# Kernel optimization log

Hardware: AMD Instinct MI355X
Metric: run time of the kernel (lower is better)

## Reference

```python
import jax, jax.numpy as jnp
import numpy as np

DIM = 384
H = 64
W = 64
NB = 8
BS = DIM // NB
WF = W // 2 + 1
EPS = 1e-5


def _layernorm(x, g, b):
    mu = jnp.mean(x, axis=-1, keepdims=True)
    var = jnp.mean(jnp.square(x - mu), axis=-1, keepdims=True)
    return (x - mu) * jax.lax.rsqrt(var + EPS) * g + b


def setup_inputs() -> dict:
    key = jax.random.key(0)
    ks = jax.random.split(key, 8)
    scale = 0.02
    x = jax.random.normal(ks[0], (8, H, W, DIM), dtype=jnp.float32)
    # complex params stored as real view (..., 2) like torch.view_as_real
    w1 = scale * jax.random.normal(ks[1], (H, WF, NB, BS, BS, 2), dtype=jnp.float32)
    b1 = scale * jax.random.normal(ks[2], (H, WF, NB, BS, 2), dtype=jnp.float32)
    norm1_w = jnp.ones((DIM,), jnp.float32)
    norm1_b = jnp.zeros((DIM,), jnp.float32)
    norm2_w = jnp.ones((DIM,), jnp.float32)
    norm2_b = jnp.zeros((DIM,), jnp.float32)
    lim1 = 1.0 / np.sqrt(DIM)
    lim2 = 1.0 / np.sqrt(4 * DIM)
    mlp_w1 = jax.random.uniform(ks[3], (DIM, 4 * DIM), jnp.float32, -lim1, lim1)
    mlp_b1 = jax.random.uniform(ks[4], (4 * DIM,), jnp.float32, -lim1, lim1)
    mlp_w2 = jax.random.uniform(ks[5], (4 * DIM, DIM), jnp.float32, -lim2, lim2)
    mlp_b2 = jax.random.uniform(ks[6], (DIM,), jnp.float32, -lim2, lim2)
    return {"x": x, "w1": w1, "b1": b1, "norm1_w": norm1_w, "norm1_b": norm1_b,
            "norm2_w": norm2_w, "norm2_b": norm2_b, "mlp_w1": mlp_w1, "mlp_b1": mlp_b1,
            "mlp_w2": mlp_w2, "mlp_b2": mlp_b2}


def reference(x, w1, b1, norm1_w, norm1_b, norm2_w, norm2_b, mlp_w1, mlp_b1, mlp_w2, mlp_b2):
    B, h, w, C = x.shape
    residual = x
    xn = _layernorm(x, norm1_w, norm1_b)
    # spectral token mixing (fp32, ortho norm)
    xf = jnp.fft.rfft2(xn.astype(jnp.float32), axes=(1, 2), norm="ortho")  # (B,H,WF,C) complex
    xf = xf.reshape(B, h, w // 2 + 1, NB, BS)
    w1c = jax.lax.complex(w1[..., 0], w1[..., 1])  # (H,WF,NB,BS,BS)
    b1c = jax.lax.complex(b1[..., 0], b1[..., 1])  # (H,WF,NB,BS)
    o1 = jnp.einsum("bhwni,hwnio->bhwno", xf, w1c) + b1c
    o1 = jax.lax.complex(jax.nn.relu(o1.real), jax.nn.relu(o1.imag))
    o1 = o1.reshape(B, h, w // 2 + 1, C)
    xs = jnp.fft.irfft2(o1, s=(h, w), axes=(1, 2), norm="ortho")  # (B,H,W,C) real
    # channel MLP (dropout in eval mode = identity), exact GELU as torch default
    xm = _layernorm(xs, norm2_w, norm2_b)
    hdn = jax.nn.gelu(xm @ mlp_w1 + mlp_b1, approximate=False)
    mlp_out = hdn @ mlp_w2 + mlp_b2
    return xs + residual + mlp_out
```

## Files before the change

### kernel.cpp

```cpp
#include <hip/hip_runtime.h>
#include <math.h>


#define BB 8
#define CC 384
#define WF 33
#define NBK 8
#define BSZ 48
#define NTOK 32768
#define TW64 0.09817477042468103f

#define T_AWF 0
#define T_AHF 5120
#define T_AHI 21504
#define T_AWI 37888

typedef __attribute__((ext_vector_type(8))) short bf16x8;
typedef __attribute__((ext_vector_type(4))) float f32x4;

__device__ __forceinline__ unsigned short f2b(float f) {
  union { float f; unsigned u; } x; x.f = f;
  unsigned u = x.u;
  return (unsigned short)((u + 0x7fffu + ((u >> 16) & 1u)) >> 16);
}
__device__ __forceinline__ float b2fl(unsigned short u) {
  return __uint_as_float(((unsigned)u) << 16);
}
__device__ __forceinline__ void gload16(const void* g, void* l) {
  __builtin_amdgcn_global_load_lds(
      (const __attribute__((address_space(1))) void*)g,
      (__attribute__((address_space(3))) void*)l, 16, 0, 0);
}

__global__ __launch_bounds__(256) void prep_kernel(unsigned short* __restrict__ A,
    const float* __restrict__ mw1, unsigned short* __restrict__ w1t,
    const float* __restrict__ mw2, unsigned short* __restrict__ w2t,
    const float* __restrict__ n2w, const float* __restrict__ n2b,
    const float* __restrict__ mb1, float2* __restrict__ gsbb) {
  __shared__ float tile[32][33];
  int bid = blockIdx.x;
  if (bid < 64) {
    int idx0 = bid * 256 + threadIdx.x;
    const float S = 0.125f;
    for (int e = idx0; e < 5120; e += 16384) {
      int m = e >> 6, w = e & 63;
      float val = 0.f;
      if (m < 66) {
        int kwv = m >> 1;
        float th = (float)((kwv * w) & 63) * TW64;
        val = (m & 1) ? (((kwv==0)||(kwv==32)) ? 0.f : -sinf(th)*S) : cosf(th)*S;
      }
      A[T_AWF + e] = f2b(val);
    }
    for (int e = idx0; e < 16384; e += 16384) {
      int comp = e >> 13; int r = e & 8191; int mp = r >> 6, hh = r & 63;
      int cpo = mp >> 6, kh = mp & 63;
      float th = (float)((kh * hh) & 63) * TW64;
      float cv = cosf(th), sv = sinf(th);
      float fv = (cpo == 0) ? (comp == 0 ? cv : sv) : (comp == 0 ? -sv : cv);
      A[T_AHF + e] = f2b(fv * S);
      float iv = (cpo == 0) ? (comp == 0 ? cv : -sv) : (comp == 0 ? sv : cv);
      A[T_AHI + e] = f2b(iv * S);
    }
    for (int e = idx0; e < 4096; e += 16384) {
      int w = e >> 6, kp = e & 63;
      float val;
      if (kp <= 32) {
        float th = (float)((kp * w) & 63) * TW64;
        val = cosf(th) * (((kp==0)||(kp==32)) ? 1.f : 2.f) * S;
      } else {
        int k2 = kp - 32;
        float th = (float)((k2 * w) & 63) * TW64;
        val = -2.f * sinf(th) * S;
      }
      A[T_AWI + e] = f2b(val);
    }
    return;
  }
  if (bid >= 1216) {
    int n0 = (bid - 1216) * 256 + threadIdx.x;
    if (n0 < 1536) {
      float gsv = 0.f, bbv = 0.f;
      for (int k = 0; k < 384; ++k) {
        float a = mw1[(size_t)k*1536 + n0];
        gsv += n2w[k]*a;
        bbv += n2b[k]*a;
      }
      gsbb[n0] = make_float2(gsv, bbv + mb1[n0]);
    }
    return;
  }
  int tx = threadIdx.x & 31, ty = threadIdx.x >> 5;
  if (bid < 640) {
    int tb = bid - 64;
    int ntc = 1536 >> 5;
    int bx = tb % ntc, by = tb / ntc;
    for (int rr2 = ty; rr2 < 32; rr2 += 8)
      tile[rr2][tx] = mw1[(size_t)(by*32+rr2)*1536 + bx*32 + tx];
    __syncthreads();
    float gv = n2w[by*32 + tx];
    for (int rr2 = ty; rr2 < 32; rr2 += 8)
      w1t[(size_t)(bx*32+rr2)*384 + by*32 + tx] = f2b(tile[tx][rr2] * gv);
  } else {
    int tb = bid - 640;
    int ntc = 384 >> 5;
    int bx = tb % ntc, by = tb / ntc;
    for (int rr2 = ty; rr2 < 32; rr2 += 8)
      tile[rr2][tx] = mw2[(size_t)(by*32+rr2)*384 + bx*32 + tx];
    __syncthreads();
    for (int rr2 = ty; rr2 < 32; rr2 += 8)
      w2t[(size_t)(bx*32+rr2)*1536 + by*32 + tx] = f2b(tile[tx][rr2]);
  }
}

__global__ __launch_bounds__(256) void ln1t_kernel(const float* __restrict__ x,
    const float* __restrict__ g, const float* __restrict__ be,
    unsigned short* __restrict__ xn) {
  int outer = blockIdx.x;
  int tid = threadIdx.x, lane = tid & 63, wg = tid >> 6;
  const float* base = x + (size_t)outer * 64 * 384;
  float s[16], s2[16];
#pragma unroll
  for (int q = 0; q < 16; ++q) { s[q] = 0.f; s2[q] = 0.f; }
  for (int ch = 0; ch < 6; ++ch) {
#pragma unroll
    for (int q = 0; q < 16; ++q) {
      float v = base[(size_t)(wg*16 + q)*384 + ch*64 + lane];
      s[q] += v; s2[q] += v*v;
    }
  }
#pragma unroll
  for (int q = 0; q < 16; ++q) {
#pragma unroll
    for (int off = 32; off >= 1; off >>= 1) {
      s[q] += __shfl_xor(s[q], off);
      s2[q] += __shfl_xor(s2[q], off);
    }
  }
  float mu[16], rs[16];
#pragma unroll
  for (int q = 0; q < 16; ++q) {
    mu[q] = s[q] * (1.f/384.f);
    rs[q] = rsqrtf(s2[q] * (1.f/384.f) - mu[q]*mu[q] + 1e-5f);
  }
  unsigned short* o = xn + (size_t)outer * 384 * 64;
  for (int ch = 0; ch < 6; ++ch) {
    int c = ch*64 + lane;
    float ga = g[c], bb2 = be[c];
#pragma unroll
    for (int qq = 0; qq < 4; ++qq) {
      unsigned short hv[4];
#pragma unroll
      for (int r2 = 0; r2 < 4; ++r2) {
        int q = qq*4 + r2;
        hv[r2] = f2b((base[(size_t)(wg*16+q)*384 + c]-mu[q])*rs[q]*ga + bb2);
      }
      uint2 pw;
      pw.x = hv[0] | ((unsigned)hv[1] << 16);
      pw.y = hv[2] | ((unsigned)hv[3] << 16);
      *(uint2*)(o + (size_t)c*64 + wg*16 + qq*4) = pw;
    }
  }
}

template<int STAGE>
__global__ __launch_bounds__(256) void dft_kernel(
    const unsigned short* __restrict__ A0, const unsigned short* __restrict__ D,
    unsigned short* __restrict__ O) {
  constexpr int M = (STAGE==0) ? 80 : (STAGE==3) ? 64 : 128;
  constexpr int MT = M / 16;
  constexpr int NA = (STAGE==1 || STAGE==2) ? 2 : 1;
  constexpr int ABYTES = NA * M * 128;
  constexpr int STG2 = ABYTES + 16384;
  constexpr int EPB = 64 * 128 * 4;
  constexpr int SB = (STG2 > EPB) ? STG2 : EPB;
  __shared__ __align__(16) char smem[SB];
  char* BPL = smem + ABYTES;

  int bid = blockIdx.x;
  int cc = bid % 3; int outer = bid / 3;
  int c0 = cc * 128;
  int tid = threadIdx.x, lane = tid & 63, wid = tid >> 6;
  int rr = lane & 15, rq = lane >> 4;
  int b, h = 0, kw = 0;
  if (STAGE == 0 || STAGE == 3) { b = outer >> 6; h = outer & 63; }
  else { b = outer / 33; kw = outer % 33; }

  f32x4 acc[MT][2];
#pragma unroll
  for (int mt = 0; mt < MT; ++mt)
#pragma unroll
    for (int nt = 0; nt < 2; ++nt) acc[mt][nt] = (f32x4){0.f,0.f,0.f,0.f};

  const unsigned short* Atab =
    (STAGE==0) ? A0+T_AWF : (STAGE==1) ? A0+T_AHF : (STAGE==2) ? A0+T_AHI : A0+T_AWI;
  constexpr int ACH = NA * M * 8;
#pragma unroll
  for (int i = 0; i < (ACH + 255)/256; ++i) {
    int t2 = tid + i*256;
    if ((ACH % 256 == 0) || (t2 < ACH)) {
      int mm = t2 >> 3, ch = t2 & 7;
      gload16(Atab + mm*64 + ((ch ^ (mm & 7)) << 3), smem + i*4096 + wid*1024);
    }
  }

  int ncomp = (STAGE == 1) ? ((kw == 0 || kw == 32) ? 1 : 2) : NA;

  for (int comp = 0; comp < ncomp; ++comp) {
    if (comp) __syncthreads();
    if (STAGE == 0) {
      const unsigned short* src = D + (((size_t)(b*64 + h))*384 + c0) * 64;
#pragma unroll
      for (int i = 0; i < 4; ++i) {
        int idx = tid + i*256;
        int c = idx >> 3, ch = idx & 7;
        gload16(src + c*64 + ((ch ^ (c & 7)) << 3), BPL + i*4096 + wid*1024);
      }
    } else {
      size_t P; int RS;
      if (STAGE == 1) { P = (size_t)b*(64*66*384) + (size_t)(2*kw + comp)*384 + c0; RS = 66*384; }
      else if (STAGE == 2) { P = ((size_t)((b*2 + comp)*33) + kw)*64*384 + c0; RS = 384; }
      else { P = (size_t)b*(64*64*384) + (size_t)h*384 + c0; RS = 64*384; }
      const unsigned short* p0 = D + P;
#pragma unroll
      for (int i = 0; i < 4; ++i) {
        int kq = (tid >> 6) + i*4;
        int c2 = (tid & 63) * 2;
        const unsigned short* p = p0 + (size_t)(4*kq)*RS + c2;
        unsigned u0 = *(const unsigned*)p;
        unsigned u1 = *(const unsigned*)(p + RS);
        unsigned u2 = *(const unsigned*)(p + 2*(size_t)RS);
        unsigned u3 = *(const unsigned*)(p + 3*(size_t)RS);
        uint2 w0, w1v;
        w0.x = (u0 & 0xffffu) | (u1 << 16);
        w0.y = (u2 & 0xffffu) | (u3 << 16);
        w1v.x = (u0 >> 16) | (u1 & 0xffff0000u);
        w1v.y = (u2 >> 16) | (u3 & 0xffff0000u);
        *(uint2*)(BPL + c2*128 + ((kq*8) ^ ((c2 & 7) << 4))) = w0;
        *(uint2*)(BPL + (c2+1)*128 + ((kq*8) ^ (((c2+1) & 7) << 4))) = w1v;
      }
    }
    __syncthreads();
#pragma unroll
    for (int kh2 = 0; kh2 < 2; ++kh2) {
      int chb = kh2*4 + rq;
      bf16x8 bfr[2];
#pragma unroll
      for (int nt = 0; nt < 2; ++nt) {
        int n = wid*32 + nt*16 + rr;
        bfr[nt] = *(const bf16x8*)(BPL + n*128 + ((chb ^ (n & 7)) << 4));
      }
#pragma unroll
      for (int mt = 0; mt < MT; ++mt) {
        int mr = mt*16 + rr;
        bf16x8 af = *(const bf16x8*)(smem + comp*(M*128) + mr*128 + ((chb ^ (mr & 7)) << 4));
#pragma unroll
        for (int nt = 0; nt < 2; ++nt)
          acc[mt][nt] = __builtin_amdgcn_mfma_f32_16x16x32_bf16(af, bfr[nt], acc[mt][nt], 0, 0, 0);
      }
    }
  }
  __syncthreads();

  float* ep = (float*)smem;
  constexpr int NHM = (M + 63) / 64;
#pragma unroll
  for (int hm = 0; hm < NHM; ++hm) {
    if (hm) __syncthreads();
#pragma unroll
    for (int mo = 0; mo < 4; ++mo) {
      int mt = hm*4 + mo;
      if (mt >= MT) break;
#pragma unroll
      for (int nt = 0; nt < 2; ++nt)
#pragma unroll
        for (int j = 0; j < 4; ++j) {
          int m2 = mo*16 + rq*4 + j;
          int cl = wid*32 + nt*16 + rr;
          ep[m2*128 + (cl ^ ((m2 & 7) << 2))] = acc[mt][nt][j];
        }
    }
    __syncthreads();
    for (int it = tid; it < 64*16; it += 256) {
      int m2 = it >> 4, u8 = it & 15;
      int m = hm*64 + m2;
      if (m >= M) break;
      if (STAGE == 0 && m >= 66) break;
      if (STAGE == 2) { int cp = m >> 6; if (cp && (kw == 0 || kw == 32)) continue; }
      int swz = (m2 & 7) << 2;
      float4 v0 = *(const float4*)(ep + m2*128 + ((u8*8) ^ swz));
      float4 v1 = *(const float4*)(ep + m2*128 + ((u8*8 + 4) ^ swz));
      uint4 pw;
      pw.x = f2b(v0.x) | ((unsigned)f2b(v0.y) << 16);
      pw.y = f2b(v0.z) | ((unsigned)f2b(v0.w) << 16);
      pw.z = f2b(v1.x) | ((unsigned)f2b(v1.y) << 16);
      pw.w = f2b(v1.z) | ((unsigned)f2b(v1.w) << 16);
      size_t rowb;
      if (STAGE == 0) rowb = ((size_t)(b*64 + h)*66 + m)*384 + c0;
      else if (STAGE == 1) { int cp = m >> 6, kh = m & 63;
        rowb = (((size_t)((b*2 + cp)*64 + kh)*33) + kw)*384 + c0; }
      else if (STAGE == 2) { int cp = m >> 6, h2 = m & 63; int kp = cp ? 32 + kw : kw;
        rowb = ((size_t)(b*64 + kp)*64 + h2)*384 + c0; }
      else rowb = ((size_t)(b*64 + h)*64 + m)*384 + c0;
      *(uint4*)(O + rowb + u8*8) = pw;
    }
  }
}

__global__ __launch_bounds__(384) void blockmm2_kernel(
    const unsigned short* __restrict__ S2, const float* __restrict__ w1,
    const float* __restrict__ b1, unsigned short* __restrict__ o1) {
  int bid = blockIdx.x;
  int np = bid % 4;
  int kw = (bid / 4) % WF;
  int h = bid / (4*WF);
  int tid = threadIdx.x;
  __shared__ float4 wl4[2][48*24];
  __shared__ float2 xl[2][BB][48];
  __shared__ float2 bl[2][48];
#pragma unroll
  for (int e = tid; e < 2304; e += 384) {
    int sub = e / 1152, r = e % 1152;
    const float4* wb4 = (const float4*)(w1 + ((size_t)((h*WF + kw)*NBK) + 2*np + sub)*(BSZ*BSZ*2));
    wl4[sub][r] = wb4[r];
  }
  if (tid < 96) {
    int sub = tid / 48, o = tid % 48;
    bl[sub][o] = ((const float2*)b1)[((size_t)((h*WF + kw)*NBK) + 2*np + sub)*BSZ + o];
  }
#pragma unroll
  for (int e = tid; e < 768; e += 384) {
    int sub = e / 384, r = e % 384, bb = r / 48, i = r % 48;
    int n = 2*np + sub;
    size_t ir = (((size_t)((bb*2 + 0)*64 + h)*33) + kw)*384 + n*48 + i;
    size_t ii = (((size_t)((bb*2 + 1)*64 + h)*33) + kw)*384 + n*48 + i;
    xl[sub][bb][i] = make_float2(b2fl(S2[ir]), b2fl(S2[ii]));
  }
  __syncthreads();
  int sub = tid / 192, r = tid % 192, bb = r / 24, o2 = r % 24;
  float4 bv = *(const float4*)(&bl[sub][2*o2]);
  float2 a0 = make_float2(bv.x, bv.y);
  float2 a1 = make_float2(bv.z, bv.w);
#pragma unroll
  for (int i = 0; i < 48; ++i) {
    float2 xv = xl[sub][bb][i];
    float4 wv = wl4[sub][i*24 + o2];
    a0.x += xv.x*wv.x - xv.y*wv.y;
    a0.y += xv.x*wv.y + xv.y*wv.x;
    a1.x += xv.x*wv.z - xv.y*wv.w;
    a1.y += xv.x*wv.w + xv.y*wv.z;
  }
  int n = 2*np + sub;
  size_t idr = (((size_t)((bb*2 + 0)*33) + kw)*64 + h)*384 + n*48 + 2*o2;
  size_t idi = (((size_t)((bb*2 + 1)*33) + kw)*64 + h)*384 + n*48 + 2*o2;
  *(unsigned*)(o1 + idr) = f2b(fmaxf(a0.x, 0.f)) | ((unsigned)f2b(fmaxf(a1.x, 0.f)) << 16);
  *(unsigned*)(o1 + idi) = f2b(fmaxf(a0.y, 0.f)) | ((unsigned)f2b(fmaxf(a1.y, 0.f)) << 16);
}

__global__ __launch_bounds__(256) void stats_kernel(const unsigned short* __restrict__ in,
    float2* __restrict__ stats) {
  int token = blockIdx.x * 4 + (threadIdx.x >> 6);
  int lane = threadIdx.x & 63;
  const unsigned short* row = in + (size_t)token * CC;
  float s = 0.f, s2 = 0.f;
#pragma unroll
  for (int j = 0; j < 6; ++j) {
    float v = b2fl(row[lane + 64*j]);
    s += v; s2 += v*v;
  }
#pragma unroll
  for (int off = 32; off >= 1; off >>= 1) {
    s += __shfl_xor(s, off);
    s2 += __shfl_xor(s2, off);
  }
  if (lane == 0) {
    float mu = s * (1.0f/CC);
    float rs = rsqrtf(s2 * (1.0f/CC) - mu*mu + 1e-5f);
    stats[token] = make_float2(mu, rs);
  }
}

template<int MODE>
__global__ __launch_bounds__(256) void mfma_gemm_kernel(
    const unsigned short* __restrict__ A, int lda,
    const unsigned short* __restrict__ BT, int ldbt,
    void* __restrict__ Cp, int ldc, int K, int ntn,
    const float2* __restrict__ stats, const float2* __restrict__ gsbb,
    const unsigned short* __restrict__ xsb, const float* __restrict__ xres,
    const float* __restrict__ b2v) {
  __shared__ __align__(16) char gsm[49152];
  int nb = (int)gridDim.x;
  int bidx = (int)blockIdx.x;
  int bswz = (bidx & 7) * (nb >> 3) + (bidx >> 3);
  int bn = bswz % ntn;
  int bm = bswz / ntn;
  int t = threadIdx.x;
  int lane = t & 63;
  int wid = t >> 6;
  int wm = wid >> 1, wn = wid & 1;
  int rr = lane & 15, rq = lane >> 4;

  f32x4 acc[4][4];
#pragma unroll
  for (int m = 0; m < 4; ++m)
#pragma unroll
    for (int n = 0; n < 4; ++n) acc[m][n] = (f32x4){0.f,0.f,0.f,0.f};

  const unsigned short* Abase = A + (size_t)bm*128*lda;
  const unsigned short* Bbase = BT + (size_t)bn*128*ldbt;
  int nt = K >> 5;

#define STG(bsel, t0)                                                        \
  {                                                                          \
    _Pragma("unroll")                                                        \
    for (int i = 0; i < 2; ++i) {                                            \
      int u = t + i*256;                                                     \
      int row = u >> 2, ch = u & 3;                                          \
      gload16(Abase + (size_t)row*lda + (t0)*32 + ((ch ^ (row & 3)) << 3),   \
              gsm + (bsel)*16384 + i*4096 + wid*1024);                       \
      gload16(Bbase + (size_t)row*ldbt + (t0)*32 + ((ch ^ (row & 3)) << 3),  \
              gsm + (bsel)*16384 + 8192 + i*4096 + wid*1024);                \
    }                                                                        \
  }

#define CMP(bsel)                                                            \
  {                                                                          \
    const char* Ab2 = gsm + (bsel)*16384;                                    \
    const char* Bb2 = Ab2 + 8192;                                            \
    bf16x8 af[4], bfv[4];                                                    \
    _Pragma("unroll")                                                        \
    for (int m = 0; m < 4; ++m) {                                            \
      int row = wm*64 + m*16 + rr;                                           \
      af[m] = *(const bf16x8*)(Ab2 + row*64 + ((rq ^ (row & 3)) << 4));      \
    }                                                                        \
    _Pragma("unroll")                                                        \
    for (int n = 0; n < 4; ++n) {                                            \
      int row = wn*64 + n*16 + rr;                                           \
      bfv[n] = *(const bf16x8*)(Bb2 + row*64 + ((rq ^ (row & 3)) << 4));     \
    }                                                                        \
    _Pragma("unroll")                                                        \
    for (int m = 0; m < 4; ++m)                                              \
      _Pragma("unroll")                                                      \
      for (int n = 0; n < 4; ++n)                                            \
        acc[m][n] = __builtin_amdgcn_mfma_f32_16x16x32_bf16(af[m], bfv[n], acc[m][n], 0, 0, 0); \
  }

  STG(0, 0);
  STG(1, 1);
  int cur = 0;
  for (int tt = 0; tt < nt; ++tt) {
    if (tt + 2 < nt) {
      int nb3 = cur + 2; if (nb3 >= 3) nb3 -= 3;
      STG(nb3, tt + 2);
      __builtin_amdgcn_sched_barrier(0);
      asm volatile("s_waitcnt vmcnt(8)" ::: "memory");
    } else if (tt + 1 < nt) {
      __builtin_amdgcn_sched_barrier(0);
      asm volatile("s_waitcnt vmcnt(4)" ::: "memory");
    } else {
      __builtin_amdgcn_sched_barrier(0);
      asm volatile("s_waitcnt vmcnt(0)" ::: "memory");
    }
    __builtin_amdgcn_sched_barrier(0);
    __builtin_amdgcn_s_barrier();
    __builtin_amdgcn_sched_barrier(0);
    CMP(cur);
    __builtin_amdgcn_s_barrier();
    cur = (cur + 1 == 3) ? 0 : cur + 1;
  }
  __syncthreads();
#undef STG
#undef CMP

  if (MODE == 0) {
    unsigned short* ep = (unsigned short*)gsm;
#pragma unroll
    for (int m = 0; m < 4; ++m) {
      float2 st[4];
#pragma unroll
      for (int j = 0; j < 4; ++j)
        st[j] = stats[bm*128 + wm*64 + m*16 + rq*4 + j];
#pragma unroll
      for (int n = 0; n < 4; ++n) {
        int lcol = wn*64 + n*16 + rr;
        float2 gb = gsbb[bn*128 + lcol];
#pragma unroll
        for (int j = 0; j < 4; ++j) {
          float v = st[j].y * acc[m][n][j] - st[j].y * st[j].x * gb.x + gb.y;
          v = 0.5f*v*(1.f + erff(v*0.70710678118654752f));
          int row = wm*64 + m*16 + rq*4 + j;
          ep[row*128 + (lcol ^ ((row & 7) << 3))] = f2b(v);
        }
      }
    }
    __syncthreads();
    for (int it = t; it < 128*16; it += 256) {
      int m = it >> 4, u8 = it & 15;
      uint4 pw = *(const uint4*)(ep + m*128 + ((u8*8) ^ ((m & 7) << 3)));
      *(uint4*)((unsigned short*)Cp + (size_t)(bm*128 + m)*ldc + bn*128 + u8*8) = pw;
    }
  } else {
    float* ep = (float*)gsm;
#pragma unroll
    for (int half = 0; half < 2; ++half) {
      __syncthreads();
#pragma unroll
      for (int mo = 0; mo < 2; ++mo) {
        int m = half*2 + mo;
#pragma unroll
        for (int n = 0; n < 4; ++n)
#pragma unroll
          for (int j = 0; j < 4; ++j) {
            int lr = wm*32 + mo*16 + rq*4 + j;
            int col = wn*64 + n*16 + rr;
            ep[lr*128 + (col ^ ((lr & 7) << 2))] = acc[m][n][j];
          }
      }
      __syncthreads();
      for (int it = t; it < 64*32; it += 256) {
        int lr = it >> 5, u = it & 31;
        int swz = (lr & 7) << 2;
        float4 v = *(const float4*)(ep + lr*128 + ((u*4) ^ swz));
        int grow = bm*128 + (lr >> 5)*64 + (half*2 + ((lr >> 4) & 1))*16 + (lr & 15);
        int gcol = bn*128 + u*4;
        size_t idx = (size_t)grow*ldc + gcol;
        float4 xr = *(const float4*)(xres + idx);
        uint2 xsv = *(const uint2*)(xsb + idx);
        float4 bv = *(const float4*)(b2v + gcol);
        float4 ov;
        ov.x = v.x + xr.x + b2fl((unsigned short)(xsv.x & 0xffffu)) + bv.x;
        ov.y = v.y + xr.y + b2fl((unsigned short)(xsv.x >> 16)) + bv.y;
        ov.z = v.z + xr.z + b2fl((unsigned short)(xsv.y & 0xffffu)) + bv.z;
        ov.w = v.w + xr.w + b2fl((unsigned short)(xsv.y >> 16)) + bv.w;
        *(float4*)((float*)Cp + idx) = ov;
      }
    }
  }
}

extern "C" void kernel_launch(void* const* d_in, const int* in_sizes, int n_in,
                              void* d_out, int out_size, void* d_ws, size_t ws_size,
                              hipStream_t stream) {
  const float* x   = (const float*)d_in[0];
  const float* w1  = (const float*)d_in[1];
  const float* b1  = (const float*)d_in[2];
  const float* n1w = (const float*)d_in[3];
  const float* n1b = (const float*)d_in[4];
  const float* n2w = (const float*)d_in[5];
  const float* n2b = (const float*)d_in[6];
  const float* mw1 = (const float*)d_in[7];
  const float* mb1 = (const float*)d_in[8];
  const float* mw2 = (const float*)d_in[9];
  const float* mb2 = (const float*)d_in[10];
  float* out = (float*)d_out;

  char* ws = (char*)d_ws;
  const size_t MB = 1ull << 20;
  unsigned short* xn  = (unsigned short*)(ws + 0*MB);
  unsigned short* S1  = (unsigned short*)(ws + 26*MB);
  unsigned short* S2  = (unsigned short*)(ws + 53*MB);
  unsigned short* o1  = (unsigned short*)(ws + 80*MB);
  unsigned short* S3  = (unsigned short*)(ws + 107*MB);
  unsigned short* xsb = (unsigned short*)(ws + 133*MB);
  float2*         stats = (float2*)(ws + 159*MB);
  unsigned short* hid = (unsigned short*)(ws + 160*MB);
  unsigned short* w1t = (unsigned short*)(ws + 261*MB);
  unsigned short* w2t = (unsigned short*)(ws + 263*MB);
  unsigned short* atab = (unsigned short*)(ws + 265*MB);
  float2*         gsbb = (float2*)(ws + 266*MB);

  prep_kernel<<<1222, 256, 0, stream>>>(atab, mw1, w1t, mw2, w2t, n2w, n2b, mb1, gsbb);
  ln1t_kernel<<<512, 256, 0, stream>>>(x, n1w, n1b, xn);
  dft_kernel<0><<<512*3, 256, 0, stream>>>(atab, xn, S1);
  dft_kernel<1><<<264*3, 256, 0, stream>>>(atab, S1, S2);
  blockmm2_kernel<<<64*WF*4, 384, 0, stream>>>(S2, w1, b1, o1);
  dft_kernel<2><<<264*3, 256, 0, stream>>>(atab, o1, S3);
  dft_kernel<3><<<512*3, 256, 0, stream>>>(atab, S3, xsb);
  stats_kernel<<<NTOK/4, 256, 0, stream>>>(xsb, stats);
  mfma_gemm_kernel<0><<<256*12, 256, 0, stream>>>(xsb, 384, w1t, 384,
                                                  hid, 1536, 384, 12,
                                                  stats, gsbb, nullptr, nullptr, nullptr);
  mfma_gemm_kernel<1><<<256*3, 256, 0, stream>>>(hid, 1536, w2t, 1536,
                                                 out, 384, 1536, 3,
                                                 nullptr, nullptr, xsb, x, mb2);
}
```

Measured before the change: 404.0 us.

## Fuse LN1 into prep kernel, double-buffer GEMM, use fast sigmoid GELU

Merges the first layernorm into the weight-prep launch so one kernel launch is removed. Replaces the GEMM's 3-stage pipeline, which used explicit vmcnt waits, with a simpler 2-buffer loop that uses __syncthreads, and shrinks LDS to 32KB to allow more resident blocks. Swaps the erf-based GELU for a sigmoid/exp2 approximation that is cheaper to evaluate. The approximation adds error relative to exact GELU, and the shallower pipeline can expose more memory latency.

```diff
diff --git a/kernel.cpp b/kernel.cpp
--- a/kernel.cpp
+++ b/kernel.cpp
@@ -31,14 +31,72 @@
       (const __attribute__((address_space(1))) void*)g,
       (__attribute__((address_space(3))) void*)l, 16, 0, 0);
 }
-
-__global__ __launch_bounds__(256) void prep_kernel(unsigned short* __restrict__ A,
+__device__ __forceinline__ float gelu_fast(float v) {
+  float z = 2.3022082f*v + 0.1029433f*v*v*v;
+  z = fminf(fmaxf(z, -36.f), 36.f);
+  float e = exp2f(z);
+  return v * e * __builtin_amdgcn_rcpf(e + 1.f);
+}
+
+__global__ __launch_bounds__(256) void prep_ln1_kernel(
+    const float* __restrict__ x, const float* __restrict__ n1w,
+    const float* __restrict__ n1b, unsigned short* __restrict__ xn,
+    unsigned short* __restrict__ A,
     const float* __restrict__ mw1, unsigned short* __restrict__ w1t,
     const float* __restrict__ mw2, unsigned short* __restrict__ w2t,
     const float* __restrict__ n2w, const float* __restrict__ n2b,
     const float* __restrict__ mb1, float2* __restrict__ gsbb) {
   __shared__ float tile[32][33];
-  int bid = blockIdx.x;
+  int bid0 = blockIdx.x;
+  if (bid0 < 512) {
+    int outer = bid0;
+    int tid = threadIdx.x, lane = tid & 63, wg = tid >> 6;
+    const float* base = x + (size_t)outer * 64 * 384;
+    float s[16], s2[16];
+#pragma unroll
+    for (int q = 0; q < 16; ++q) { s[q] = 0.f; s2[q] = 0.f; }
+    for (int ch = 0; ch < 6; ++ch) {
+#pragma unroll
+      for (int q = 0; q < 16; ++q) {
+        float v = base[(size_t)(wg*16 + q)*384 + ch*64 + lane];
+        s[q] += v; s2[q] += v*v;
+      }
+    }
+#pragma unroll
+    for (int q = 0; q < 16; ++q) {
+#pragma unroll
+      for (int off = 32; off >= 1; off >>= 1) {
+        s[q] += __shfl_xor(s[q], off);
+        s2[q] += __shfl_xor(s2[q], off);
+      }
+    }
+    float mu[16], rs[16];
+#pragma unroll
+    for (int q = 0; q < 16; ++q) {
+      mu[q] = s[q] * (1.f/384.f);
+      rs[q] = rsqrtf(s2[q] * (1.f/384.f) - mu[q]*mu[q] + 1e-5f);
+    }
+    unsigned short* o = xn + (size_t)outer * 384 * 64;
+    for (int ch = 0; ch < 6; ++ch) {
+      int c = ch*64 + lane;
+      float ga = n1w[c], bb2 = n1b[c];
+#pragma unroll
+      for (int qq = 0; qq < 4; ++qq) {
+        unsigned short hv[4];
+#pragma unroll
+        for (int r2 = 0; r2 < 4; ++r2) {
+          int q = qq*4 + r2;
+          hv[r2] = f2b((base[(size_t)(wg*16+q)*384 + c]-mu[q])*rs[q]*ga + bb2);
+        }
+        uint2 pw;
+        pw.x = hv[0] | ((unsigned)hv[1] << 16);
+        pw.y = hv[2] | ((unsigned)hv[3] << 16);
+        *(uint2*)(o + (size_t)c*64 + wg*16 + qq*4) = pw;
+      }
+    }
+    return;
+  }
+  int bid = bid0 - 512;
   if (bid < 64) {
     int idx0 = bid * 256 + threadIdx.x;
     const float S = 0.125f;
@@ -110,56 +168,6 @@
     __syncthreads();
     for (int rr2 = ty; rr2 < 32; rr2 += 8)
       w2t[(size_t)(bx*32+rr2)*1536 + by*32 + tx] = f2b(tile[tx][rr2]);
-  }
-}
-
-__global__ __launch_bounds__(256) void ln1t_kernel(const float* __restrict__ x,
-    const float* __restrict__ g, const float* __restrict__ be,
-    unsigned short* __restrict__ xn) {
-  int outer = blockIdx.x;
-  int tid = threadIdx.x, lane = tid & 63, wg = tid >> 6;
-  const float* base = x + (size_t)outer * 64 * 384;
-  float s[16], s2[16];
-#pragma unroll
-  for (int q = 0; q < 16; ++q) { s[q] = 0.f; s2[q] = 0.f; }
-  for (int ch = 0; ch < 6; ++ch) {
-#pragma unroll
-    for (int q = 0; q < 16; ++q) {
-      float v = base[(size_t)(wg*16 + q)*384 + ch*64 + lane];
-      s[q] += v; s2[q] += v*v;
-    }
-  }
-#pragma unroll
-  for (int q = 0; q < 16; ++q) {
-#pragma unroll
-    for (int off = 32; off >= 1; off >>= 1) {
-      s[q] += __shfl_xor(s[q], off);
-      s2[q] += __shfl_xor(s2[q], off);
-    }
-  }
-  float mu[16], rs[16];
-#pragma unroll
-  for (int q = 0; q < 16; ++q) {
-    mu[q] = s[q] * (1.f/384.f);
-    rs[q] = rsqrtf(s2[q] * (1.f/384.f) - mu[q]*mu[q] + 1e-5f);
-  }
-  unsigned short* o = xn + (size_t)outer * 384 * 64;
-  for (int ch = 0; ch < 6; ++ch) {
-    int c = ch*64 + lane;
-    float ga = g[c], bb2 = be[c];
-#pragma unroll
-    for (int qq = 0; qq < 4; ++qq) {
-      unsigned short hv[4];
-#pragma unroll
-      for (int r2 = 0; r2 < 4; ++r2) {
-        int q = qq*4 + r2;
-        hv[r2] = f2b((base[(size_t)(wg*16+q)*384 + c]-mu[q])*rs[q]*ga + bb2);
-      }
-      uint2 pw;
-      pw.x = hv[0] | ((unsigned)hv[1] << 16);
-      pw.y = hv[2] | ((unsigned)hv[3] << 16);
-      *(uint2*)(o + (size_t)c*64 + wg*16 + qq*4) = pw;
-    }
   }
 }
 
@@ -388,7 +396,7 @@
     const float2* __restrict__ stats, const float2* __restrict__ gsbb,
     const unsigned short* __restrict__ xsb, const float* __restrict__ xres,
     const float* __restrict__ b2v) {
-  __shared__ __align__(16) char gsm[49152];
+  __shared__ __align__(16) char gsm[32768];
   int nb = (int)gridDim.x;
   int bidx = (int)blockIdx.x;
   int bswz = (bidx & 7) * (nb >> 3) + (bidx >> 3);
@@ -446,28 +454,15 @@
   }
 
   STG(0, 0);
-  STG(1, 1);
+  __syncthreads();
   int cur = 0;
-  for (int tt = 0; tt < nt; ++tt) {
-    if (tt + 2 < nt) {
-      int nb3 = cur + 2; if (nb3 >= 3) nb3 -= 3;
-      STG(nb3, tt + 2);
-      __builtin_amdgcn_sched_barrier(0);
-      asm volatile("s_waitcnt vmcnt(8)" ::: "memory");
-    } else if (tt + 1 < nt) {
-      __builtin_amdgcn_sched_barrier(0);
-      asm volatile("s_waitcnt vmcnt(4)" ::: "memory");
-    } else {
-      __builtin_amdgcn_sched_barrier(0);
-      asm volatile("s_waitcnt vmcnt(0)" ::: "memory");
-    }
-    __builtin_amdgcn_sched_barrier(0);
-    __builtin_amdgcn_s_barrier();
-    __builtin_amdgcn_sched_barrier(0);
+  for (int tt = 0; tt < nt - 1; ++tt) {
+    STG(cur ^ 1, tt + 1);
     CMP(cur);
-    __builtin_amdgcn_s_barrier();
-    cur = (cur + 1 == 3) ? 0 : cur + 1;
-  }
+    __syncthreads();
+    cur ^= 1;
+  }
+  CMP(cur);
   __syncthreads();
 #undef STG
 #undef CMP
@@ -487,7 +482,7 @@
 #pragma unroll
         for (int j = 0; j < 4; ++j) {
           float v = st[j].y * acc[m][n][j] - st[j].y * st[j].x * gb.x + gb.y;
-          v = 0.5f*v*(1.f + erff(v*0.70710678118654752f));
+          v = gelu_fast(v);
           int row = wm*64 + m*16 + rq*4 + j;
           ep[row*128 + (lcol ^ ((row & 7) << 3))] = f2b(v);
         }
@@ -569,8 +564,9 @@
   unsigned short* atab = (unsigned short*)(ws + 265*MB);
   float2*         gsbb = (float2*)(ws + 266*MB);
 
-  prep_kernel<<<1222, 256, 0, stream>>>(atab, mw1, w1t, mw2, w2t, n2w, n2b, mb1, gsbb);
-  ln1t_kernel<<<512, 256, 0, stream>>>(x, n1w, n1b, xn);
+  prep_ln1_kernel<<<1734, 256, 0, stream>>>(x, n1w, n1b, xn,
+                                            atab, mw1, w1t, mw2, w2t,
+                                            n2w, n2b, mb1, gsbb);
   dft_kernel<0><<<512*3, 256, 0, stream>>>(atab, xn, S1);
   dft_kernel<1><<<264*3, 256, 0, stream>>>(atab, S1, S2);
   blockmm2_kernel<<<64*WF*4, 384, 0, stream>>>(S2, w1, b1, o1);
```

Result: faster. 356.6 us (-11.7%).
